# Optimization experiments

Measured on AMD Instinct MI355X. Metric: run time of the kernel, lower is better.

Reference implementation:

```python
import jax, jax.numpy as jnp
import numpy as np

N_NODES = 100_000
N_EDGES = 1_600_000
N_GRAPHS = 512
IN_C, HID_C, OUT_C = 17, 64, 32


def setup_inputs() -> dict:
    key = jax.random.key(0)
    ks = jax.random.split(key, 12)
    x = jax.random.normal(ks[0], (N_NODES, IN_C), dtype=jnp.float32)
    edge_index = jax.random.randint(ks[1], (2, N_EDGES), 0, N_NODES, dtype=jnp.int64)
    batch = jnp.sort(jax.random.randint(ks[2], (N_NODES,), 0, N_GRAPHS, dtype=jnp.int64))
    def lin(k, fan_in, fan_out):
        s = 1.0 / np.sqrt(fan_in)
        kw, kb = jax.random.split(k)
        W = jax.random.uniform(kw, (fan_in, fan_out), minval=-s, maxval=s, dtype=jnp.float32)
        b = jax.random.uniform(kb, (fan_out,), minval=-s, maxval=s, dtype=jnp.float32)
        return W, b
    W1, b1 = lin(ks[3], IN_C, HID_C)      # GCNConv 1
    W2, b2 = lin(ks[4], HID_C, OUT_C)     # GCNConv 2
    Wf1, bf1 = lin(ks[5], OUT_C, OUT_C)   # fc1
    Wf2, bf2 = lin(ks[6], OUT_C, OUT_C)   # fc2
    return {"x": x, "edge_index": edge_index, "batch": batch,
            "W1": W1, "b1": b1, "W2": W2, "b2": b2,
            "Wf1": Wf1, "bf1": bf1, "Wf2": Wf2, "bf2": bf2}


def _gcn_conv(x, src, dst, norm, W, b, n_nodes):
    # PyG GCNConv: h = x @ W; out_i = sum_{j->i} norm_ij * h_j; out += bias
    h = x @ W                                   # [N, d_out]
    msg = h[src] * norm[:, None]                # gather + scale [E+N, d_out]
    out = jax.ops.segment_sum(msg, dst, num_segments=n_nodes)
    return out + b


def reference(x, edge_index, batch, W1, b1, W2, b2, Wf1, bf1, Wf2, bf2):
    n = x.shape[0]
    loops = jnp.arange(n, dtype=edge_index.dtype)
    src = jnp.concatenate([edge_index[0], loops])  # add self loops
    dst = jnp.concatenate([edge_index[1], loops])
    # symmetric normalization: deg^-1/2[src] * deg^-1/2[dst]
    deg = jax.ops.segment_sum(jnp.ones_like(dst, dtype=x.dtype), dst, num_segments=n)
    dinv = jnp.where(deg > 0, 1.0 / jnp.sqrt(deg), 0.0)
    norm = dinv[src] * dinv[dst]

    h = jax.nn.relu(_gcn_conv(x, src, dst, norm, W1, b1, n))
    h = _gcn_conv(h, src, dst, norm, W2, b2, n)

    # global mean pool over graphs
    cnt = jax.ops.segment_sum(jnp.ones((n,), dtype=h.dtype), batch, num_segments=N_GRAPHS)
    pooled = jax.ops.segment_sum(h, batch, num_segments=N_GRAPHS) / jnp.clip(cnt, 1.0)[:, None]

    out = jax.nn.relu(pooled @ Wf1 + bf1)
    out = out @ Wf2 + bf2
    return out  # [N_GRAPHS, OUT_C]
```

## Files before the change

### kernel.cpp

```cpp
#include <hip/hip_runtime.h>

#define IN_C 17
#define HID  64
#define OUTC 32

#define CH   8192
#define TA   512
#define NBP  512
#define BCAP 5632
#define BS_BLKS 8

typedef __attribute__((ext_vector_type(2))) float f2;
typedef __attribute__((ext_vector_type(8))) short bf16x8;
typedef __attribute__((ext_vector_type(4))) float f32x4;
__device__ __forceinline__ f2 mkf2(float x, float y) { f2 r; r.x = x; r.y = y; return r; }

__device__ __forceinline__ unsigned short f2bf(float f) {
    unsigned u = __float_as_uint(f);
    u += 0x7fffu + ((u >> 16) & 1u);
    return (unsigned short)(u >> 16);
}
__device__ __forceinline__ float bflo(unsigned u) { return __uint_as_float(u << 16); }
__device__ __forceinline__ float bfhi(unsigned u) { return __uint_as_float(u & 0xffff0000u); }

__global__ __launch_bounds__(TA) void k_binA(const int* __restrict__ src,
        const int* __restrict__ dst, int E,
        int* __restrict__ outbuf, int* __restrict__ cntmat, int* __restrict__ offmat) {
    __shared__ int cnt[NBP];
    __shared__ int off[NBP];
    __shared__ int stage[CH];
    int t = threadIdx.x;
    long base = (long)blockIdx.x * CH;
    int nE = (int)(E - base); if (nE > CH) nE = CH;
    cnt[t] = 0;
    __syncthreads();
    int bk[16], pk[16], rk[16];
#pragma unroll
    for (int j = 0; j < 16; ++j) {
        int idx = t + j * TA;
        if (idx < nE) {
            long e = base + idx;
            int d = __builtin_nontemporal_load(&dst[e]);
            int s = __builtin_nontemporal_load(&src[e]);
            int b = d >> 8;
            bk[j] = b;
            pk[j] = s | ((d & 255) << 17);
            rk[j] = atomicAdd(&cnt[b], 1);
        } else bk[j] = -1;
    }
    __syncthreads();
    int c = cnt[t];
    off[t] = c;
    __syncthreads();
    int inc = c;
    for (int s = 1; s < NBP; s <<= 1) {
        int add = (t >= s) ? off[t - s] : 0;
        __syncthreads();
        inc += add; off[t] = inc;
        __syncthreads();
    }
    int excl = inc - c;
    __syncthreads();
    off[t] = excl;
    __syncthreads();
#pragma unroll
    for (int j = 0; j < 16; ++j)
        if (bk[j] >= 0) stage[off[bk[j]] + rk[j]] = pk[j];
    __syncthreads();
    for (int i = t; i < nE; i += TA) outbuf[base + i] = stage[i];
    cntmat[blockIdx.x * NBP + t] = c;
    offmat[blockIdx.x * NBP + t] = excl;
}

__global__ __launch_bounds__(NBP) void k_bsum1(const int* __restrict__ cntmat,
        int nblkA, int* __restrict__ part, float* __restrict__ pool, int poolN) {
    int t = threadIdx.x, b = blockIdx.x;
    int per = (nblkA + BS_BLKS - 1) / BS_BLKS;
    int i0 = b * per, i1 = min(i0 + per, nblkA);
    int s = 0;
    for (int i = i0; i < i1; ++i) s += cntmat[i * NBP + t];
    part[b * NBP + t] = s;
    for (int i = b * NBP + t; i < poolN; i += BS_BLKS * NBP) pool[i] = 0.f;
}

__global__ __launch_bounds__(NBP) void k_bsum2(const int* __restrict__ part,
        int* __restrict__ bbase, const float* __restrict__ W2,
        uint4* __restrict__ w2frag) {
    __shared__ int sh[NBP];
    int t = threadIdx.x;
    int s = 0;
#pragma unroll
    for (int i = 0; i < BS_BLKS; ++i) s += part[i * NBP + t];
    sh[t] = s;
    __syncthreads();
    int inc = s;
    for (int st = 1; st < NBP; st <<= 1) {
        int add = (t >= st) ? sh[t - st] : 0;
        __syncthreads();
        inc += add; sh[t] = inc;
        __syncthreads();
    }
    bbase[t] = inc - s;
    if (t < 256) {
        int f = t >> 6, l = t & 63;
        int kt = f >> 1, nt = f & 1;
        int kbase = kt * 32 + (l >> 4) * 8;
        int c = nt * 16 + (l & 15);
        unsigned short v[8];
#pragma unroll
        for (int j = 0; j < 8; ++j) v[j] = f2bf(W2[(kbase + j) * OUTC + c]);
        uint4 o;
        o.x = (unsigned)v[0] | ((unsigned)v[1] << 16);
        o.y = (unsigned)v[2] | ((unsigned)v[3] << 16);
        o.z = (unsigned)v[4] | ((unsigned)v[5] << 16);
        o.w = (unsigned)v[6] | ((unsigned)v[7] << 16);
        w2frag[f * 64 + l] = o;
    }
}

__global__ __launch_bounds__(TA) void k_binB(const int* __restrict__ outbuf,
        const int* __restrict__ cntmat, const int* __restrict__ offmat,
        const int* __restrict__ bbase, int nblkA, int N,
        int* __restrict__ csr, int2* __restrict__ meta,
        const float* __restrict__ x, unsigned* __restrict__ xs16h,
        unsigned short* __restrict__ xs17h) {
    __shared__ int segc[256], sego[256], segs[256];
    __shared__ int ndeg[256], noff[256];
    __shared__ int stage[BCAP];
    int t = threadIdx.x, b = blockIdx.x;
    if (t < 256) {
        int cc = 0, ss = 0;
        if (t < nblkA) { cc = cntmat[t * NBP + b]; ss = offmat[t * NBP + b]; }
        segc[t] = cc; segs[t] = ss; sego[t] = cc;
        ndeg[t] = 0;
    }
    __syncthreads();
    {
        int c = (t < 256) ? sego[t] : 0;
        int inc = c;
        for (int s = 1; s < 256; s <<= 1) {
            int add = (t < 256 && t >= s) ? sego[t - s] : 0;
            __syncthreads();
            if (t < 256) { inc += add; sego[t] = inc; }
            __syncthreads();
        }
        if (t < 256) sego[t] = inc - c;
    }
    __syncthreads();
    int wave = t >> 6, lane = t & 63;
    for (int i = wave; i < nblkA; i += TA / 64) {
        int c = segc[i], so = sego[i];
        long gs = (long)i * CH + segs[i];
        for (int l = lane; l < c; l += 64) {
            int p = so + l;
            if (p < BCAP) stage[p] = __builtin_nontemporal_load(&outbuf[gs + l]);
        }
    }
    __syncthreads();
    int T = sego[255] + segc[255];
    if (T > BCAP) T = BCAP;
    int mypk[11], myrk[11], ne = 0;
    for (int k = t; k < T; k += TA) {
        int p = stage[k];
        int l = (p >> 17) & 255;
        myrk[ne] = atomicAdd(&ndeg[l], 1);
        mypk[ne] = p;
        ne++;
    }
    __syncthreads();
    {
        int c = (t < 256) ? ndeg[t] : 0;
        if (t < 256) noff[t] = c;
        __syncthreads();
        int inc = c;
        for (int s = 1; s < 256; s <<= 1) {
            int add = (t < 256 && t >= s) ? noff[t - s] : 0;
            __syncthreads();
            if (t < 256) { inc += add; noff[t] = inc; }
            __syncthreads();
        }
        if (t < 256) noff[t] = inc - c;
    }
    __syncthreads();
    int gb = bbase[b];
    int n0 = b << 8;
    if (t < 256 && n0 + t < N) {
        int n = n0 + t;
        meta[n] = make_int2(gb + noff[t], ndeg[t]);
        float dinv = rsqrtf((float)(ndeg[t] + 1));
        const float* xr = x + (size_t)n * IN_C;
        unsigned* xo = xs16h + (size_t)n * 8;
#pragma unroll
        for (int w2 = 0; w2 < 8; ++w2) {
            unsigned lo = f2bf(xr[2 * w2] * dinv);
            unsigned hi = f2bf(xr[2 * w2 + 1] * dinv);
            xo[w2] = lo | (hi << 16);
        }
        xs17h[n] = f2bf(xr[16] * dinv);
    }
    for (int j = 0; j < ne; ++j) {
        int p = mypk[j];
        int l = (p >> 17) & 255;
        csr[gb + noff[l] + myrk[j]] = p & 0x1FFFF;
    }
}

__global__ __launch_bounds__(256) void k_gather1(
        const uint4* __restrict__ xs16v, const unsigned short* __restrict__ xs17h,
        const int* __restrict__ csr, const int2* __restrict__ meta,
        const float* __restrict__ W1, const float* __restrict__ b1,
        const uint4* __restrict__ w2frag, unsigned char* __restrict__ hs2b, int N) {
    __shared__ __align__(16) float aggx[16][20];
    __shared__ float dinv_sh[16];
    __shared__ __align__(16) float h1sh[16][68];

    int tid = threadIdx.x;
    int n0 = blockIdx.x * 16;
    int ch = tid & 63;
    float w1r[IN_C];
#pragma unroll
    for (int k = 0; k < IN_C; ++k) w1r[k] = W1[k * HID + ch];
    float b1v = b1[ch];

    int ln = tid >> 4, sl = tid & 15;
    int n = n0 + ln;
    f2 acc[8];
#pragma unroll
    for (int j = 0; j < 8; ++j) acc[j] = mkf2(0.f, 0.f);
    float a17 = 0.f;
    if (n < N) {
        int2 m = meta[n];
        int start = m.x, cnt = m.y, end = start + cnt;
        auto body = [&](int s) {
            uint4 v0 = xs16v[(size_t)s * 2];
            uint4 v1 = xs16v[(size_t)s * 2 + 1];
            acc[0] += mkf2(bflo(v0.x), bfhi(v0.x));
            acc[1] += mkf2(bflo(v0.y), bfhi(v0.y));
            acc[2] += mkf2(bflo(v0.z), bfhi(v0.z));
            acc[3] += mkf2(bflo(v0.w), bfhi(v0.w));
            acc[4] += mkf2(bflo(v1.x), bfhi(v1.x));
            acc[5] += mkf2(bflo(v1.y), bfhi(v1.y));
            acc[6] += mkf2(bflo(v1.z), bfhi(v1.z));
            acc[7] += mkf2(bflo(v1.w), bfhi(v1.w));
            a17 += bflo((unsigned)xs17h[s]);
        };
        for (int k = start + sl; k < end; k += 16)
            body(__builtin_nontemporal_load(&csr[k]));
        if (sl == 0) {
            body(n);
            dinv_sh[ln] = rsqrtf((float)(cnt + 1));
        }
    }
    float a[16];
#pragma unroll
    for (int j = 0; j < 8; ++j) { a[2 * j] = acc[j].x; a[2 * j + 1] = acc[j].y; }
#pragma unroll
    for (int j = 0; j < 8; ++j) {
        float tt = (sl & 8) ? a[j + 8] : a[j];
        float uu = (sl & 8) ? a[j] : a[j + 8];
        a[j] = tt + __shfl_xor(uu, 8);
    }
#pragma unroll
    for (int j = 0; j < 4; ++j) {
        float tt = (sl & 4) ? a[j + 4] : a[j];
        float uu = (sl & 4) ? a[j] : a[j + 4];
        a[j] = tt + __shfl_xor(uu, 4);
    }
#pragma unroll
    for (int j = 0; j < 2; ++j) {
        float tt = (sl & 2) ? a[j + 2] : a[j];
        float uu = (sl & 2) ? a[j] : a[j + 2];
        a[j] = tt + __shfl_xor(uu, 2);
    }
    {
        float tt = (sl & 1) ? a[1] : a[0];
        float uu = (sl & 1) ? a[0] : a[1];
        a[0] = tt + __shfl_xor(uu, 1);
    }
    a17 += __shfl_xor(a17, 1);
    a17 += __shfl_xor(a17, 2);
    a17 += __shfl_xor(a17, 4);
    a17 += __shfl_xor(a17, 8);
    aggx[ln][sl] = a[0];
    if (sl == 0) aggx[ln][16] = a17;
    __syncthreads();
    int s0 = tid >> 6;
#pragma unroll
    for (int rep = 0; rep < 4; ++rep) {
        int slot = s0 + rep * 4;
        int nn = n0 + slot;
        if (nn < N) {
            const float4* ap = (const float4*)aggx[slot];
            float4 A0 = ap[0], A1 = ap[1], A2 = ap[2], A3 = ap[3];
            float a16 = aggx[slot][16];
            float dot = A0.x * w1r[0]  + A0.y * w1r[1]  + A0.z * w1r[2]  + A0.w * w1r[3]
                      + A1.x * w1r[4]  + A1.y * w1r[5]  + A1.z * w1r[6]  + A1.w * w1r[7]
                      + A2.x * w1r[8]  + A2.y * w1r[9]  + A2.z * w1r[10] + A2.w * w1r[11]
                      + A3.x * w1r[12] + A3.y * w1r[13] + A3.z * w1r[14] + A3.w * w1r[15]
                      + a16  * w1r[16];
            float dv = dinv_sh[slot];
            h1sh[slot][ch] = dv * fmaxf(dv * dot + b1v, 0.f);
        }
    }
    __syncthreads();
    int wv = tid >> 6, l = tid & 63;
    if (wv < 2) {
        int row = l & 15, kq = l >> 4;
        const float4* hp = (const float4*)&h1sh[row][kq * 8];
        float4 f0v = hp[0], f1v = hp[1];
        const float4* hq = (const float4*)&h1sh[row][32 + kq * 8];
        float4 g0v = hq[0], g1v = hq[1];
        bf16x8 a0, a1;
        a0[0] = (short)f2bf(f0v.x); a0[1] = (short)f2bf(f0v.y);
        a0[2] = (short)f2bf(f0v.z); a0[3] = (short)f2bf(f0v.w);
        a0[4] = (short)f2bf(f1v.x); a0[5] = (short)f2bf(f1v.y);
        a0[6] = (short)f2bf(f1v.z); a0[7] = (short)f2bf(f1v.w);
        a1[0] = (short)f2bf(g0v.x); a1[1] = (short)f2bf(g0v.y);
        a1[2] = (short)f2bf(g0v.z); a1[3] = (short)f2bf(g0v.w);
        a1[4] = (short)f2bf(g1v.x); a1[5] = (short)f2bf(g1v.y);
        a1[6] = (short)f2bf(g1v.z); a1[7] = (short)f2bf(g1v.w);
        bf16x8 bA = *(const bf16x8*)&w2frag[(0 + wv) * 64 + l];
        bf16x8 bB = *(const bf16x8*)&w2frag[(2 + wv) * 64 + l];
        f32x4 d = {0.f, 0.f, 0.f, 0.f};
        d = __builtin_amdgcn_mfma_f32_16x16x32_bf16(a0, bA, d, 0, 0, 0);
        d = __builtin_amdgcn_mfma_f32_16x16x32_bf16(a1, bB, d, 0, 0, 0);
        int rbase = (l >> 4) * 4;
#pragma unroll
        for (int r = 0; r < 4; ++r) {
            int node = n0 + rbase + r;
            if (node < N) {
                unsigned pk = (unsigned)__builtin_amdgcn_cvt_pk_fp8_f32(d[r], 0.f, 0, false);
                hs2b[(size_t)node * 32 + wv * 16 + (l & 15)] = (unsigned char)(pk & 0xFFu);
            }
        }
    }
}

__global__ __launch_bounds__(256) void k_gather2(
        const uint4* __restrict__ hs2v, const int* __restrict__ csr,
        const int2* __restrict__ meta, const float* __restrict__ b2,
        const int* __restrict__ batch, float* pool, float* cntg, int N) {
    __shared__ __align__(16) float cont[16][OUTC];
    __shared__ int bsh[16];
    int tid = threadIdx.x;
    int n0 = blockIdx.x * 16;

    int ln = tid >> 4, sl = tid & 15;
    int n = n0 + ln;
    f2 acc[16];
#pragma unroll
    for (int j = 0; j < 16; ++j) acc[j] = mkf2(0.f, 0.f);
    float dinv = 0.f;
    if (n < N) {
        int2 m = meta[n];
        int start = m.x, cnt = m.y, end = start + cnt;
        dinv = rsqrtf((float)(cnt + 1));
        auto body = [&](int s) {
            const uint4* rp = hs2v + (size_t)s * 2;
            uint4 v0 = rp[0], v1 = rp[1];
            f2 t;
            t = __builtin_amdgcn_cvt_pk_f32_fp8((int)v0.x, false); acc[0]  += t;
            t = __builtin_amdgcn_cvt_pk_f32_fp8((int)v0.x, true);  acc[1]  += t;
            t = __builtin_amdgcn_cvt_pk_f32_fp8((int)v0.y, false); acc[2]  += t;
            t = __builtin_amdgcn_cvt_pk_f32_fp8((int)v0.y, true);  acc[3]  += t;
            t = __builtin_amdgcn_cvt_pk_f32_fp8((int)v0.z, false); acc[4]  += t;
            t = __builtin_amdgcn_cvt_pk_f32_fp8((int)v0.z, true);  acc[5]  += t;
            t = __builtin_amdgcn_cvt_pk_f32_fp8((int)v0.w, false); acc[6]  += t;
            t = __builtin_amdgcn_cvt_pk_f32_fp8((int)v0.w, true);  acc[7]  += t;
            t = __builtin_amdgcn_cvt_pk_f32_fp8((int)v1.x, false); acc[8]  += t;
            t = __builtin_amdgcn_cvt_pk_f32_fp8((int)v1.x, true);  acc[9]  += t;
            t = __builtin_amdgcn_cvt_pk_f32_fp8((int)v1.y, false); acc[10] += t;
            t = __builtin_amdgcn_cvt_pk_f32_fp8((int)v1.y, true);  acc[11] += t;
            t = __builtin_amdgcn_cvt_pk_f32_fp8((int)v1.z, false); acc[12] += t;
            t = __builtin_amdgcn_cvt_pk_f32_fp8((int)v1.z, true);  acc[13] += t;
            t = __builtin_amdgcn_cvt_pk_f32_fp8((int)v1.w, false); acc[14] += t;
            t = __builtin_amdgcn_cvt_pk_f32_fp8((int)v1.w, true);  acc[15] += t;
        };
        for (int k = start + sl; k < end; k += 16)
            body(__builtin_nontemporal_load(&csr[k]));
        if (sl == 0) body(n);
    }
    float a[32];
#pragma unroll
    for (int j = 0; j < 16; ++j) { a[2 * j] = acc[j].x; a[2 * j + 1] = acc[j].y; }
#pragma unroll
    for (int j = 0; j < 16; ++j) {
        float tt = (sl & 8) ? a[j + 16] : a[j];
        float uu = (sl & 8) ? a[j] : a[j + 16];
        a[j] = tt + __shfl_xor(uu, 8);
    }
#pragma unroll
    for (int j = 0; j < 8; ++j) {
        float tt = (sl & 4) ? a[j + 8] : a[j];
        float uu = (sl & 4) ? a[j] : a[j + 8];
        a[j] = tt + __shfl_xor(uu, 4);
    }
#pragma unroll
    for (int j = 0; j < 4; ++j) {
        float tt = (sl & 2) ? a[j + 4] : a[j];
        float uu = (sl & 2) ? a[j] : a[j + 4];
        a[j] = tt + __shfl_xor(uu, 2);
    }
#pragma unroll
    for (int j = 0; j < 2; ++j) {
        float tt = (sl & 1) ? a[j + 2] : a[j];
        float uu = (sl & 1) ? a[j] : a[j + 2];
        a[j] = tt + __shfl_xor(uu, 1);
    }
    if (n < N) {
        float c0 = dinv * a[0] + b2[2 * sl];
        float c1 = dinv * a[1] + b2[2 * sl + 1];
        *(float2*)&cont[ln][2 * sl] = make_float2(c0, c1);
        if (sl == 0) bsh[ln] = batch[n];
    } else {
        *(float2*)&cont[ln][2 * sl] = make_float2(0.f, 0.f);
        if (sl == 0) bsh[ln] = -1;
    }
    __syncthreads();
    if (tid < OUTC) {
        int c = tid;
        float run = 0.f; int cur = -1;
        for (int j = 0; j < 16; ++j) {
            int bj = bsh[j];
            if (bj < 0) continue;
            if (bj == cur) run += cont[j][c];
            else {
                if (cur >= 0) atomicAdd(&pool[(size_t)cur * OUTC + c], run);
                cur = bj; run = cont[j][c];
            }
        }
        if (cur >= 0) atomicAdd(&pool[(size_t)cur * OUTC + c], run);
        if (c == 0) {
            float crun = 0.f; cur = -1;
            for (int j = 0; j < 16; ++j) {
                int bj = bsh[j];
                if (bj < 0) continue;
                if (bj == cur) crun += 1.f;
                else {
                    if (cur >= 0) atomicAdd(&cntg[cur], crun);
                    cur = bj; crun = 1.f;
                }
            }
            if (cur >= 0) atomicAdd(&cntg[cur], crun);
        }
    }
}

__global__ void k_final(const float* __restrict__ pool, const float* __restrict__ cntg,
                        const float* __restrict__ Wf1, const float* __restrict__ bf1,
                        const float* __restrict__ Wf2, const float* __restrict__ bf2,
                        float* out, int G) {
    __shared__ float p[OUTC], t[OUTC];
    int g = blockIdx.x;
    int c = threadIdx.x;
    float csafe = fmaxf(cntg[g], 1.0f);
    p[c] = pool[g * OUTC + c] / csafe;
    __syncthreads();
    float acc = bf1[c];
#pragma unroll
    for (int k = 0; k < OUTC; ++k) acc += p[k] * Wf1[k * OUTC + c];
    t[c] = fmaxf(acc, 0.f);
    __syncthreads();
    float acc2 = bf2[c];
#pragma unroll
    for (int k = 0; k < OUTC; ++k) acc2 += t[k] * Wf2[k * OUTC + c];
    out[g * OUTC + c] = acc2;
}

extern "C" void kernel_launch(void* const* d_in, const int* in_sizes, int n_in,
                              void* d_out, int out_size, void* d_ws, size_t ws_size,
                              hipStream_t stream) {
    const float* x    = (const float*)d_in[0];
    const int*   ei   = (const int*)  d_in[1];
    const int*   batch= (const int*)  d_in[2];
    const float* W1   = (const float*)d_in[3];
    const float* b1   = (const float*)d_in[4];
    const float* W2   = (const float*)d_in[5];
    const float* b2   = (const float*)d_in[6];
    const float* Wf1  = (const float*)d_in[7];
    const float* bf1  = (const float*)d_in[8];
    const float* Wf2  = (const float*)d_in[9];
    const float* bf2  = (const float*)d_in[10];

    const int N = in_sizes[0] / IN_C;
    const int E = in_sizes[1] / 2;
    const int G = out_size / OUTC;
    const int* src = ei;
    const int* dst = ei + E;

    const int nblkA = (E + CH - 1) / CH;
    const int NB    = (N + 255) >> 8;

    char* w = (char*)d_ws;
    int*   csr      = (int*)w;   w += (size_t)E * sizeof(int);
    int2*  meta     = (int2*)w;  w += (size_t)N * sizeof(int2);
    unsigned* xs16h = (unsigned*)w; w += (size_t)N * 8 * sizeof(unsigned);
    unsigned char* hs2 = (unsigned char*)w; w += (size_t)N * 32;
    unsigned short* xs17h = (unsigned short*)w; w += (size_t)N * sizeof(unsigned short);
    w = (char*)(((size_t)w + 15) & ~(size_t)15);
    float* pool     = (float*)w; w += (size_t)G * OUTC * sizeof(float);
    float* cntg     = (float*)w; w += (size_t)G * sizeof(float);
    w = (char*)(((size_t)w + 15) & ~(size_t)15);
    int*   outbuf   = (int*)w;   w += (size_t)E * sizeof(int);
    int*   cntmat   = (int*)w;   w += (size_t)nblkA * NBP * sizeof(int);
    int*   offmat   = (int*)w;   w += (size_t)nblkA * NBP * sizeof(int);
    int*   bbase    = (int*)w;   w += NBP * sizeof(int);
    int*   part     = (int*)w;   w += BS_BLKS * NBP * sizeof(int);
    w = (char*)(((size_t)w + 15) & ~(size_t)15);
    uint4* w2frag   = (uint4*)w; w += 4 * 64 * sizeof(uint4);

    const int poolN = G * OUTC + G;

    k_binA<<<nblkA, TA, 0, stream>>>(src, dst, E, outbuf, cntmat, offmat);
    k_bsum1<<<BS_BLKS, NBP, 0, stream>>>(cntmat, nblkA, part, pool, poolN);
    k_bsum2<<<1, NBP, 0, stream>>>(part, bbase, W2, w2frag);
    k_binB<<<NB, TA, 0, stream>>>(outbuf, cntmat, offmat, bbase, nblkA, N,
                                  csr, meta, x, xs16h, xs17h);

    dim3 blk(256);
    k_gather1<<<(N + 15) / 16, blk, 0, stream>>>((const uint4*)xs16h, xs17h, csr, meta,
                                                 W1, b1, w2frag, hs2, N);

    k_gather2<<<(N + 15) / 16, blk, 0, stream>>>((const uint4*)hs2, csr, meta,
                                                 b2, batch, pool, cntg, N);

    k_final<<<G, OUTC, 0, stream>>>(pool, cntg, Wf1, bf1, Wf2, bf2, (float*)d_out, G);
}
```

Before: 121.1 us.

## Fold bucket-sum kernels into binning kernels and make gather kernels persistent

Removes the two small bucket-prefix kernels. Pool zeroing and W2 fragment packing move into k_binA, and each k_binB block computes its global base by summing cntmat columns for all lower buckets and reducing in shared memory. The gather kernels become grid-stride loops over 16-node tiles with a grid capped at 2048 blocks, so W1/W2 register loads are amortized across tiles. This trades two launches and their serialization for redundant column sums in every binB block (up to 196x391 reads per block) and fewer resident blocks to hide gather latency.

```diff
diff --git a/kernel.cpp b/kernel.cpp
--- a/kernel.cpp
+++ b/kernel.cpp
@@ -8,7 +8,7 @@
 #define TA   512
 #define NBP  512
 #define BCAP 5632
-#define BS_BLKS 8
+#define MAXG 2048
 
 typedef __attribute__((ext_vector_type(2))) float f2;
 typedef __attribute__((ext_vector_type(8))) short bf16x8;
@@ -25,11 +25,30 @@
 
 __global__ __launch_bounds__(TA) void k_binA(const int* __restrict__ src,
         const int* __restrict__ dst, int E,
-        int* __restrict__ outbuf, int* __restrict__ cntmat, int* __restrict__ offmat) {
+        int* __restrict__ outbuf, int* __restrict__ cntmat, int* __restrict__ offmat,
+        const float* __restrict__ W2, uint4* __restrict__ w2frag,
+        float* __restrict__ pool, int poolN) {
     __shared__ int cnt[NBP];
     __shared__ int off[NBP];
     __shared__ int stage[CH];
     int t = threadIdx.x;
+    for (int i = (int)(blockIdx.x * TA + t); i < poolN; i += (int)(gridDim.x * TA))
+        pool[i] = 0.f;
+    if (blockIdx.x == 0 && t < 256) {
+        int f = t >> 6, l = t & 63;
+        int kt = f >> 1, nt = f & 1;
+        int kbase = kt * 32 + (l >> 4) * 8;
+        int c = nt * 16 + (l & 15);
+        unsigned short v[8];
+#pragma unroll
+        for (int j = 0; j < 8; ++j) v[j] = f2bf(W2[(kbase + j) * OUTC + c]);
+        uint4 o;
+        o.x = (unsigned)v[0] | ((unsigned)v[1] << 16);
+        o.y = (unsigned)v[2] | ((unsigned)v[3] << 16);
+        o.z = (unsigned)v[4] | ((unsigned)v[5] << 16);
+        o.w = (unsigned)v[6] | ((unsigned)v[7] << 16);
+        w2frag[f * 64 + l] = o;
+    }
     long base = (long)blockIdx.x * CH;
     int nE = (int)(E - base); if (nE > CH) nE = CH;
     cnt[t] = 0;
@@ -72,62 +91,21 @@
     offmat[blockIdx.x * NBP + t] = excl;
 }
 
-__global__ __launch_bounds__(NBP) void k_bsum1(const int* __restrict__ cntmat,
-        int nblkA, int* __restrict__ part, float* __restrict__ pool, int poolN) {
-    int t = threadIdx.x, b = blockIdx.x;
-    int per = (nblkA + BS_BLKS - 1) / BS_BLKS;
-    int i0 = b * per, i1 = min(i0 + per, nblkA);
-    int s = 0;
-    for (int i = i0; i < i1; ++i) s += cntmat[i * NBP + t];
-    part[b * NBP + t] = s;
-    for (int i = b * NBP + t; i < poolN; i += BS_BLKS * NBP) pool[i] = 0.f;
-}
-
-__global__ __launch_bounds__(NBP) void k_bsum2(const int* __restrict__ part,
-        int* __restrict__ bbase, const float* __restrict__ W2,
-        uint4* __restrict__ w2frag) {
-    __shared__ int sh[NBP];
-    int t = threadIdx.x;
-    int s = 0;
-#pragma unroll
-    for (int i = 0; i < BS_BLKS; ++i) s += part[i * NBP + t];
-    sh[t] = s;
-    __syncthreads();
-    int inc = s;
-    for (int st = 1; st < NBP; st <<= 1) {
-        int add = (t >= st) ? sh[t - st] : 0;
-        __syncthreads();
-        inc += add; sh[t] = inc;
-        __syncthreads();
-    }
-    bbase[t] = inc - s;
-    if (t < 256) {
-        int f = t >> 6, l = t & 63;
-        int kt = f >> 1, nt = f & 1;
-        int kbase = kt * 32 + (l >> 4) * 8;
-        int c = nt * 16 + (l & 15);
-        unsigned short v[8];
-#pragma unroll
-        for (int j = 0; j < 8; ++j) v[j] = f2bf(W2[(kbase + j) * OUTC + c]);
-        uint4 o;
-        o.x = (unsigned)v[0] | ((unsigned)v[1] << 16);
-        o.y = (unsigned)v[2] | ((unsigned)v[3] << 16);
-        o.z = (unsigned)v[4] | ((unsigned)v[5] << 16);
-        o.w = (unsigned)v[6] | ((unsigned)v[7] << 16);
-        w2frag[f * 64 + l] = o;
-    }
-}
-
 __global__ __launch_bounds__(TA) void k_binB(const int* __restrict__ outbuf,
         const int* __restrict__ cntmat, const int* __restrict__ offmat,
-        const int* __restrict__ bbase, int nblkA, int N,
+        int nblkA, int N,
         int* __restrict__ csr, int2* __restrict__ meta,
         const float* __restrict__ x, unsigned* __restrict__ xs16h,
         unsigned short* __restrict__ xs17h) {
     __shared__ int segc[256], sego[256], segs[256];
     __shared__ int ndeg[256], noff[256];
+    __shared__ int red[TA];
     __shared__ int stage[BCAP];
     int t = threadIdx.x, b = blockIdx.x;
+    int colsum = 0;
+    if (t < b) {
+        for (int i = 0; i < nblkA; ++i) colsum += cntmat[i * NBP + t];
+    }
     if (t < 256) {
         int cc = 0, ss = 0;
         if (t < nblkA) { cc = cntmat[t * NBP + b]; ss = offmat[t * NBP + b]; }
@@ -182,7 +160,13 @@
         if (t < 256) noff[t] = inc - c;
     }
     __syncthreads();
-    int gb = bbase[b];
+    red[t] = colsum;
+    __syncthreads();
+    for (int s = TA / 2; s > 0; s >>= 1) {
+        if (t < s) red[t] += red[t + s];
+        __syncthreads();
+    }
+    int gb = red[0];
     int n0 = b << 8;
     if (t < 256 && n0 + t < N) {
         int n = n0 + t;
@@ -209,240 +193,248 @@
         const uint4* __restrict__ xs16v, const unsigned short* __restrict__ xs17h,
         const int* __restrict__ csr, const int2* __restrict__ meta,
         const float* __restrict__ W1, const float* __restrict__ b1,
-        const uint4* __restrict__ w2frag, unsigned char* __restrict__ hs2b, int N) {
+        const uint4* __restrict__ w2frag, unsigned char* __restrict__ hs2b,
+        int N, int ntiles) {
     __shared__ __align__(16) float aggx[16][20];
     __shared__ float dinv_sh[16];
     __shared__ __align__(16) float h1sh[16][68];
 
     int tid = threadIdx.x;
-    int n0 = blockIdx.x * 16;
     int ch = tid & 63;
     float w1r[IN_C];
 #pragma unroll
     for (int k = 0; k < IN_C; ++k) w1r[k] = W1[k * HID + ch];
     float b1v = b1[ch];
-
+    int wv = tid >> 6, l = tid & 63;
+    bf16x8 bA = *(const bf16x8*)&w2frag[(0 + (wv & 1)) * 64 + l];
+    bf16x8 bB = *(const bf16x8*)&w2frag[(2 + (wv & 1)) * 64 + l];
     int ln = tid >> 4, sl = tid & 15;
-    int n = n0 + ln;
-    f2 acc[8];
-#pragma unroll
-    for (int j = 0; j < 8; ++j) acc[j] = mkf2(0.f, 0.f);
-    float a17 = 0.f;
-    if (n < N) {
-        int2 m = meta[n];
-        int start = m.x, cnt = m.y, end = start + cnt;
-        auto body = [&](int s) {
-            uint4 v0 = xs16v[(size_t)s * 2];
-            uint4 v1 = xs16v[(size_t)s * 2 + 1];
-            acc[0] += mkf2(bflo(v0.x), bfhi(v0.x));
-            acc[1] += mkf2(bflo(v0.y), bfhi(v0.y));
-            acc[2] += mkf2(bflo(v0.z), bfhi(v0.z));
-            acc[3] += mkf2(bflo(v0.w), bfhi(v0.w));
-            acc[4] += mkf2(bflo(v1.x), bfhi(v1.x));
-            acc[5] += mkf2(bflo(v1.y), bfhi(v1.y));
-            acc[6] += mkf2(bflo(v1.z), bfhi(v1.z));
-            acc[7] += mkf2(bflo(v1.w), bfhi(v1.w));
-            a17 += bflo((unsigned)xs17h[s]);
-        };
-        for (int k = start + sl; k < end; k += 16)
-            body(__builtin_nontemporal_load(&csr[k]));
-        if (sl == 0) {
-            body(n);
-            dinv_sh[ln] = rsqrtf((float)(cnt + 1));
-        }
-    }
-    float a[16];
-#pragma unroll
-    for (int j = 0; j < 8; ++j) { a[2 * j] = acc[j].x; a[2 * j + 1] = acc[j].y; }
-#pragma unroll
-    for (int j = 0; j < 8; ++j) {
-        float tt = (sl & 8) ? a[j + 8] : a[j];
-        float uu = (sl & 8) ? a[j] : a[j + 8];
-        a[j] = tt + __shfl_xor(uu, 8);
-    }
-#pragma unroll
-    for (int j = 0; j < 4; ++j) {
-        float tt = (sl & 4) ? a[j + 4] : a[j];
-        float uu = (sl & 4) ? a[j] : a[j + 4];
-        a[j] = tt + __shfl_xor(uu, 4);
-    }
-#pragma unroll
-    for (int j = 0; j < 2; ++j) {
-        float tt = (sl & 2) ? a[j + 2] : a[j];
-        float uu = (sl & 2) ? a[j] : a[j + 2];
-        a[j] = tt + __shfl_xor(uu, 2);
-    }
-    {
-        float tt = (sl & 1) ? a[1] : a[0];
-        float uu = (sl & 1) ? a[0] : a[1];
-        a[0] = tt + __shfl_xor(uu, 1);
-    }
-    a17 += __shfl_xor(a17, 1);
-    a17 += __shfl_xor(a17, 2);
-    a17 += __shfl_xor(a17, 4);
-    a17 += __shfl_xor(a17, 8);
-    aggx[ln][sl] = a[0];
-    if (sl == 0) aggx[ln][16] = a17;
-    __syncthreads();
     int s0 = tid >> 6;
-#pragma unroll
-    for (int rep = 0; rep < 4; ++rep) {
-        int slot = s0 + rep * 4;
-        int nn = n0 + slot;
-        if (nn < N) {
-            const float4* ap = (const float4*)aggx[slot];
-            float4 A0 = ap[0], A1 = ap[1], A2 = ap[2], A3 = ap[3];
-            float a16 = aggx[slot][16];
-            float dot = A0.x * w1r[0]  + A0.y * w1r[1]  + A0.z * w1r[2]  + A0.w * w1r[3]
-                      + A1.x * w1r[4]  + A1.y * w1r[5]  + A1.z * w1r[6]  + A1.w * w1r[7]
-                      + A2.x * w1r[8]  + A2.y * w1r[9]  + A2.z * w1r[10] + A2.w * w1r[11]
-                      + A3.x * w1r[12] + A3.y * w1r[13] + A3.z * w1r[14] + A3.w * w1r[15]
-                      + a16  * w1r[16];
-            float dv = dinv_sh[slot];
-            h1sh[slot][ch] = dv * fmaxf(dv * dot + b1v, 0.f);
-        }
-    }
-    __syncthreads();
-    int wv = tid >> 6, l = tid & 63;
-    if (wv < 2) {
-        int row = l & 15, kq = l >> 4;
-        const float4* hp = (const float4*)&h1sh[row][kq * 8];
-        float4 f0v = hp[0], f1v = hp[1];
-        const float4* hq = (const float4*)&h1sh[row][32 + kq * 8];
-        float4 g0v = hq[0], g1v = hq[1];
-        bf16x8 a0, a1;
-        a0[0] = (short)f2bf(f0v.x); a0[1] = (short)f2bf(f0v.y);
-        a0[2] = (short)f2bf(f0v.z); a0[3] = (short)f2bf(f0v.w);
-        a0[4] = (short)f2bf(f1v.x); a0[5] = (short)f2bf(f1v.y);
-        a0[6] = (short)f2bf(f1v.z); a0[7] = (short)f2bf(f1v.w);
-        a1[0] = (short)f2bf(g0v.x); a1[1] = (short)f2bf(g0v.y);
-        a1[2] = (short)f2bf(g0v.z); a1[3] = (short)f2bf(g0v.w);
-        a1[4] = (short)f2bf(g1v.x); a1[5] = (short)f2bf(g1v.y);
-        a1[6] = (short)f2bf(g1v.z); a1[7] = (short)f2bf(g1v.w);
-        bf16x8 bA = *(const bf16x8*)&w2frag[(0 + wv) * 64 + l];
-        bf16x8 bB = *(const bf16x8*)&w2frag[(2 + wv) * 64 + l];
-        f32x4 d = {0.f, 0.f, 0.f, 0.f};
-        d = __builtin_amdgcn_mfma_f32_16x16x32_bf16(a0, bA, d, 0, 0, 0);
-        d = __builtin_amdgcn_mfma_f32_16x16x32_bf16(a1, bB, d, 0, 0, 0);
-        int rbase = (l >> 4) * 4;
-#pragma unroll
-        for (int r = 0; r < 4; ++r) {
-            int node = n0 + rbase + r;
-            if (node < N) {
-                unsigned pk = (unsigned)__builtin_amdgcn_cvt_pk_fp8_f32(d[r], 0.f, 0, false);
-                hs2b[(size_t)node * 32 + wv * 16 + (l & 15)] = (unsigned char)(pk & 0xFFu);
+
+    for (int tile = blockIdx.x; tile < ntiles; tile += gridDim.x) {
+        int n0 = tile * 16;
+        int n = n0 + ln;
+        f2 acc[8];
+#pragma unroll
+        for (int j = 0; j < 8; ++j) acc[j] = mkf2(0.f, 0.f);
+        float a17 = 0.f;
+        if (n < N) {
+            int2 m = meta[n];
+            int start = m.x, cnt = m.y, end = start + cnt;
+            auto body = [&](int s) {
+                uint4 v0 = xs16v[(size_t)s * 2];
+                uint4 v1 = xs16v[(size_t)s * 2 + 1];
+                acc[0] += mkf2(bflo(v0.x), bfhi(v0.x));
+                acc[1] += mkf2(bflo(v0.y), bfhi(v0.y));
+                acc[2] += mkf2(bflo(v0.z), bfhi(v0.z));
+                acc[3] += mkf2(bflo(v0.w), bfhi(v0.w));
+                acc[4] += mkf2(bflo(v1.x), bfhi(v1.x));
+                acc[5] += mkf2(bflo(v1.y), bfhi(v1.y));
+                acc[6] += mkf2(bflo(v1.z), bfhi(v1.z));
+                acc[7] += mkf2(bflo(v1.w), bfhi(v1.w));
+                a17 += bflo((unsigned)xs17h[s]);
+            };
+            for (int k = start + sl; k < end; k += 16)
+                body(__builtin_nontemporal_load(&csr[k]));
+            if (sl == 0) {
+                body(n);
+                dinv_sh[ln] = rsqrtf((float)(cnt + 1));
             }
         }
+        float a[16];
+#pragma unroll
+        for (int j = 0; j < 8; ++j) { a[2 * j] = acc[j].x; a[2 * j + 1] = acc[j].y; }
+#pragma unroll
+        for (int j = 0; j < 8; ++j) {
+            float tt = (sl & 8) ? a[j + 8] : a[j];
+            float uu = (sl & 8) ? a[j] : a[j + 8];
+            a[j] = tt + __shfl_xor(uu, 8);
+        }
+#pragma unroll
+        for (int j = 0; j < 4; ++j) {
+            float tt = (sl & 4) ? a[j + 4] : a[j];
+            float uu = (sl & 4) ? a[j] : a[j + 4];
+            a[j] = tt + __shfl_xor(uu, 4);
+        }
+#pragma unroll
+        for (int j = 0; j < 2; ++j) {
+            float tt = (sl & 2) ? a[j + 2] : a[j];
+            float uu = (sl & 2) ? a[j] : a[j + 2];
+            a[j] = tt + __shfl_xor(uu, 2);
+        }
+        {
+            float tt = (sl & 1) ? a[1] : a[0];
+            float uu = (sl & 1) ? a[0] : a[1];
+            a[0] = tt + __shfl_xor(uu, 1);
+        }
+        a17 += __shfl_xor(a17, 1);
+        a17 += __shfl_xor(a17, 2);
+        a17 += __shfl_xor(a17, 4);
+        a17 += __shfl_xor(a17, 8);
+        aggx[ln][sl] = a[0];
+        if (sl == 0) aggx[ln][16] = a17;
+        __syncthreads();
+#pragma unroll
+        for (int rep = 0; rep < 4; ++rep) {
+            int slot = s0 + rep * 4;
+            int nn = n0 + slot;
+            if (nn < N) {
+                const float4* ap = (const float4*)aggx[slot];
+                float4 A0 = ap[0], A1 = ap[1], A2 = ap[2], A3 = ap[3];
+                float a16 = aggx[slot][16];
+                float dot = A0.x * w1r[0]  + A0.y * w1r[1]  + A0.z * w1r[2]  + A0.w * w1r[3]
+                          + A1.x * w1r[4]  + A1.y * w1r[5]  + A1.z * w1r[6]  + A1.w * w1r[7]
+                          + A2.x * w1r[8]  + A2.y * w1r[9]  + A2.z * w1r[10] + A2.w * w1r[11]
+                          + A3.x * w1r[12] + A3.y * w1r[13] + A3.z * w1r[14] + A3.w * w1r[15]
+                          + a16  * w1r[16];
+                float dv = dinv_sh[slot];
+                h1sh[slot][ch] = dv * fmaxf(dv * dot + b1v, 0.f);
+            }
+        }
+        __syncthreads();
+        if (wv < 2) {
+            int row = l & 15, kq = l >> 4;
+            const float4* hp = (const float4*)&h1sh[row][kq * 8];
+            float4 f0v = hp[0], f1v = hp[1];
+            const float4* hq = (const float4*)&h1sh[row][32 + kq * 8];
+            float4 g0v = hq[0], g1v = hq[1];
+            bf16x8 a0, a1;
+            a0[0] = (short)f2bf(f0v.x); a0[1] = (short)f2bf(f0v.y);
+            a0[2] = (short)f2bf(f0v.z); a0[3] = (short)f2bf(f0v.w);
+            a0[4] = (short)f2bf(f1v.x); a0[5] = (short)f2bf(f1v.y);
+            a0[6] = (short)f2bf(f1v.z); a0[7] = (short)f2bf(f1v.w);
+            a1[0] = (short)f2bf(g0v.x); a1[1] = (short)f2bf(g0v.y);
+            a1[2] = (short)f2bf(g0v.z); a1[3] = (short)f2bf(g0v.w);
+            a1[4] = (short)f2bf(g1v.x); a1[5] = (short)f2bf(g1v.y);
+            a1[6] = (short)f2bf(g1v.z); a1[7] = (short)f2bf(g1v.w);
+            f32x4 d = {0.f, 0.f, 0.f, 0.f};
+            d = __builtin_amdgcn_mfma_f32_16x16x32_bf16(a0, bA, d, 0, 0, 0);
+            d = __builtin_amdgcn_mfma_f32_16x16x32_bf16(a1, bB, d, 0, 0, 0);
+            int rbase = (l >> 4) * 4;
+#pragma unroll
+            for (int r = 0; r < 4; ++r) {
+                int node = n0 + rbase + r;
+                if (node < N) {
+                    unsigned pk = (unsigned)__builtin_amdgcn_cvt_pk_fp8_f32(d[r], 0.f, 0, false);
+                    hs2b[(size_t)node * 32 + wv * 16 + (l & 15)] = (unsigned char)(pk & 0xFFu);
+                }
+            }
+        }
+        __syncthreads();
     }
 }
 
 __global__ __launch_bounds__(256) void k_gather2(
         const uint4* __restrict__ hs2v, const int* __restrict__ csr,
         const int2* __restrict__ meta, const float* __restrict__ b2,
-        const int* __restrict__ batch, float* pool, float* cntg, int N) {
+        const int* __restrict__ batch, float* pool, float* cntg,
+        int N, int ntiles) {
     __shared__ __align__(16) float cont[16][OUTC];
     __shared__ int bsh[16];
     int tid = threadIdx.x;
-    int n0 = blockIdx.x * 16;
-
     int ln = tid >> 4, sl = tid & 15;
-    int n = n0 + ln;
-    f2 acc[16];
-#pragma unroll
-    for (int j = 0; j < 16; ++j) acc[j] = mkf2(0.f, 0.f);
-    float dinv = 0.f;
-    if (n < N) {
-        int2 m = meta[n];
-        int start = m.x, cnt = m.y, end = start + cnt;
-        dinv = rsqrtf((float)(cnt + 1));
-        auto body = [&](int s) {
-            const uint4* rp = hs2v + (size_t)s * 2;
-            uint4 v0 = rp[0], v1 = rp[1];
-            f2 t;
-            t = __builtin_amdgcn_cvt_pk_f32_fp8((int)v0.x, false); acc[0]  += t;
-            t = __builtin_amdgcn_cvt_pk_f32_fp8((int)v0.x, true);  acc[1]  += t;
-            t = __builtin_amdgcn_cvt_pk_f32_fp8((int)v0.y, false); acc[2]  += t;
-            t = __builtin_amdgcn_cvt_pk_f32_fp8((int)v0.y, true);  acc[3]  += t;
-            t = __builtin_amdgcn_cvt_pk_f32_fp8((int)v0.z, false); acc[4]  += t;
-            t = __builtin_amdgcn_cvt_pk_f32_fp8((int)v0.z, true);  acc[5]  += t;
-            t = __builtin_amdgcn_cvt_pk_f32_fp8((int)v0.w, false); acc[6]  += t;
-            t = __builtin_amdgcn_cvt_pk_f32_fp8((int)v0.w, true);  acc[7]  += t;
-            t = __builtin_amdgcn_cvt_pk_f32_fp8((int)v1.x, false); acc[8]  += t;
-            t = __builtin_amdgcn_cvt_pk_f32_fp8((int)v1.x, true);  acc[9]  += t;
-            t = __builtin_amdgcn_cvt_pk_f32_fp8((int)v1.y, false); acc[10] += t;
-            t = __builtin_amdgcn_cvt_pk_f32_fp8((int)v1.y, true);  acc[11] += t;
-            t = __builtin_amdgcn_cvt_pk_f32_fp8((int)v1.z, false); acc[12] += t;
-            t = __builtin_amdgcn_cvt_pk_f32_fp8((int)v1.z, true);  acc[13] += t;
-            t = __builtin_amdgcn_cvt_pk_f32_fp8((int)v1.w, false); acc[14] += t;
-            t = __builtin_amdgcn_cvt_pk_f32_fp8((int)v1.w, true);  acc[15] += t;
-        };
-        for (int k = start + sl; k < end; k += 16)
-            body(__builtin_nontemporal_load(&csr[k]));
-        if (sl == 0) body(n);
-    }
-    float a[32];
-#pragma unroll
-    for (int j = 0; j < 16; ++j) { a[2 * j] = acc[j].x; a[2 * j + 1] = acc[j].y; }
-#pragma unroll
-    for (int j = 0; j < 16; ++j) {
-        float tt = (sl & 8) ? a[j + 16] : a[j];
-        float uu = (sl & 8) ? a[j] : a[j + 16];
-        a[j] = tt + __shfl_xor(uu, 8);
-    }
-#pragma unroll
-    for (int j = 0; j < 8; ++j) {
-        float tt = (sl & 4) ? a[j + 8] : a[j];
-        float uu = (sl & 4) ? a[j] : a[j + 8];
-        a[j] = tt + __shfl_xor(uu, 4);
-    }
-#pragma unroll
-    for (int j = 0; j < 4; ++j) {
-        float tt = (sl & 2) ? a[j + 4] : a[j];
-        float uu = (sl & 2) ? a[j] : a[j + 4];
-        a[j] = tt + __shfl_xor(uu, 2);
-    }
-#pragma unroll
-    for (int j = 0; j < 2; ++j) {
-        float tt = (sl & 1) ? a[j + 2] : a[j];
-        float uu = (sl & 1) ? a[j] : a[j + 2];
-        a[j] = tt + __shfl_xor(uu, 1);
-    }
-    if (n < N) {
-        float c0 = dinv * a[0] + b2[2 * sl];
-        float c1 = dinv * a[1] + b2[2 * sl + 1];
-        *(float2*)&cont[ln][2 * sl] = make_float2(c0, c1);
-        if (sl == 0) bsh[ln] = batch[n];
-    } else {
-        *(float2*)&cont[ln][2 * sl] = make_float2(0.f, 0.f);
-        if (sl == 0) bsh[ln] = -1;
-    }
-    __syncthreads();
-    if (tid < OUTC) {
-        int c = tid;
-        float run = 0.f; int cur = -1;
+
+    for (int tile = blockIdx.x; tile < ntiles; tile += gridDim.x) {
+        int n0 = tile * 16;
+        int n = n0 + ln;
+        f2 acc[16];
+#pragma unroll
+        for (int j = 0; j < 16; ++j) acc[j] = mkf2(0.f, 0.f);
+        float dinv = 0.f;
+        if (n < N) {
+            int2 m = meta[n];
+            int start = m.x, cnt = m.y, end = start + cnt;
+            dinv = rsqrtf((float)(cnt + 1));
+            auto body = [&](int s) {
+                const uint4* rp = hs2v + (size_t)s * 2;
+                uint4 v0 = rp[0], v1 = rp[1];
+                f2 t;
+                t = __builtin_amdgcn_cvt_pk_f32_fp8((int)v0.x, false); acc[0]  += t;
+                t = __builtin_amdgcn_cvt_pk_f32_fp8((int)v0.x, true);  acc[1]  += t;
+                t = __builtin_amdgcn_cvt_pk_f32_fp8((int)v0.y, false); acc[2]  += t;
+                t = __builtin_amdgcn_cvt_pk_f32_fp8((int)v0.y, true);  acc[3]  += t;
+                t = __builtin_amdgcn_cvt_pk_f32_fp8((int)v0.z, false); acc[4]  += t;
+                t = __builtin_amdgcn_cvt_pk_f32_fp8((int)v0.z, true);  acc[5]  += t;
+                t = __builtin_amdgcn_cvt_pk_f32_fp8((int)v0.w, false); acc[6]  += t;
+                t = __builtin_amdgcn_cvt_pk_f32_fp8((int)v0.w, true);  acc[7]  += t;
+                t = __builtin_amdgcn_cvt_pk_f32_fp8((int)v1.x, false); acc[8]  += t;
+                t = __builtin_amdgcn_cvt_pk_f32_fp8((int)v1.x, true);  acc[9]  += t;
+                t = __builtin_amdgcn_cvt_pk_f32_fp8((int)v1.y, false); acc[10] += t;
+                t = __builtin_amdgcn_cvt_pk_f32_fp8((int)v1.y, true);  acc[11] += t;
+                t = __builtin_amdgcn_cvt_pk_f32_fp8((int)v1.z, false); acc[12] += t;
+                t = __builtin_amdgcn_cvt_pk_f32_fp8((int)v1.z, true);  acc[13] += t;
+                t = __builtin_amdgcn_cvt_pk_f32_fp8((int)v1.w, false); acc[14] += t;
+                t = __builtin_amdgcn_cvt_pk_f32_fp8((int)v1.w, true);  acc[15] += t;
+            };
+            for (int k = start + sl; k < end; k += 16)
+                body(__builtin_nontemporal_load(&csr[k]));
+            if (sl == 0) body(n);
+        }
+        float a[32];
+#pragma unroll
+        for (int j = 0; j < 16; ++j) { a[2 * j] = acc[j].x; a[2 * j + 1] = acc[j].y; }
+#pragma unroll
         for (int j = 0; j < 16; ++j) {
-            int bj = bsh[j];
-            if (bj < 0) continue;
-            if (bj == cur) run += cont[j][c];
-            else {
-                if (cur >= 0) atomicAdd(&pool[(size_t)cur * OUTC + c], run);
-                cur = bj; run = cont[j][c];
-            }
-        }
-        if (cur >= 0) atomicAdd(&pool[(size_t)cur * OUTC + c], run);
-        if (c == 0) {
-            float crun = 0.f; cur = -1;
+            float tt = (sl & 8) ? a[j + 16] : a[j];
+            float uu = (sl & 8) ? a[j] : a[j + 16];
+            a[j] = tt + __shfl_xor(uu, 8);
+        }
+#pragma unroll
+        for (int j = 0; j < 8; ++j) {
+            float tt = (sl & 4) ? a[j + 8] : a[j];
+            float uu = (sl & 4) ? a[j] : a[j + 8];
+            a[j] = tt + __shfl_xor(uu, 4);
+        }
+#pragma unroll
+        for (int j = 0; j < 4; ++j) {
+            float tt = (sl & 2) ? a[j + 4] : a[j];
+            float uu = (sl & 2) ? a[j] : a[j + 4];
+            a[j] = tt + __shfl_xor(uu, 2);
+        }
+#pragma unroll
+        for (int j = 0; j < 2; ++j) {
+            float tt = (sl & 1) ? a[j + 2] : a[j];
+            float uu = (sl & 1) ? a[j] : a[j + 2];
+            a[j] = tt + __shfl_xor(uu, 1);
+        }
+        if (n < N) {
+            float c0 = dinv * a[0] + b2[2 * sl];
+            float c1 = dinv * a[1] + b2[2 * sl + 1];
+            *(float2*)&cont[ln][2 * sl] = make_float2(c0, c1);
+            if (sl == 0) bsh[ln] = batch[n];
+        } else {
+            *(float2*)&cont[ln][2 * sl] = make_float2(0.f, 0.f);
+            if (sl == 0) bsh[ln] = -1;
+        }
+        __syncthreads();
+        if (tid < OUTC) {
+            int c = tid;
+            float run = 0.f; int cur = -1;
             for (int j = 0; j < 16; ++j) {
                 int bj = bsh[j];
                 if (bj < 0) continue;
-                if (bj == cur) crun += 1.f;
+                if (bj == cur) run += cont[j][c];
                 else {
-                    if (cur >= 0) atomicAdd(&cntg[cur], crun);
-                    cur = bj; crun = 1.f;
+                    if (cur >= 0) atomicAdd(&pool[(size_t)cur * OUTC + c], run);
+                    cur = bj; run = cont[j][c];
                 }
             }
-            if (cur >= 0) atomicAdd(&cntg[cur], crun);
-        }
+            if (cur >= 0) atomicAdd(&pool[(size_t)cur * OUTC + c], run);
+            if (c == 0) {
+                float crun = 0.f; cur = -1;
+                for (int j = 0; j < 16; ++j) {
+                    int bj = bsh[j];
+                    if (bj < 0) continue;
+                    if (bj == cur) crun += 1.f;
+                    else {
+                        if (cur >= 0) atomicAdd(&cntg[cur], crun);
+                        cur = bj; crun = 1.f;
+                    }
+                }
+                if (cur >= 0) atomicAdd(&cntg[cur], crun);
+            }
+        }
+        __syncthreads();
     }
 }
 
@@ -504,25 +496,24 @@
     int*   outbuf   = (int*)w;   w += (size_t)E * sizeof(int);
     int*   cntmat   = (int*)w;   w += (size_t)nblkA * NBP * sizeof(int);
     int*   offmat   = (int*)w;   w += (size_t)nblkA * NBP * sizeof(int);
-    int*   bbase    = (int*)w;   w += NBP * sizeof(int);
-    int*   part     = (int*)w;   w += BS_BLKS * NBP * sizeof(int);
     w = (char*)(((size_t)w + 15) & ~(size_t)15);
     uint4* w2frag   = (uint4*)w; w += 4 * 64 * sizeof(uint4);
 
     const int poolN = G * OUTC + G;
-
-    k_binA<<<nblkA, TA, 0, stream>>>(src, dst, E, outbuf, cntmat, offmat);
-    k_bsum1<<<BS_BLKS, NBP, 0, stream>>>(cntmat, nblkA, part, pool, poolN);
-    k_bsum2<<<1, NBP, 0, stream>>>(part, bbase, W2, w2frag);
-    k_binB<<<NB, TA, 0, stream>>>(outbuf, cntmat, offmat, bbase, nblkA, N,
+    const int ntiles = (N + 15) / 16;
+    const int gg = ntiles < MAXG ? ntiles : MAXG;
+
+    k_binA<<<nblkA, TA, 0, stream>>>(src, dst, E, outbuf, cntmat, offmat,
+                                     W2, w2frag, pool, poolN);
+    k_binB<<<NB, TA, 0, stream>>>(outbuf, cntmat, offmat, nblkA, N,
                                   csr, meta, x, xs16h, xs17h);
 
     dim3 blk(256);
-    k_gather1<<<(N + 15) / 16, blk, 0, stream>>>((const uint4*)xs16h, xs17h, csr, meta,
-                                                 W1, b1, w2frag, hs2, N);
-
-    k_gather2<<<(N + 15) / 16, blk, 0, stream>>>((const uint4*)hs2, csr, meta,
-                                                 b2, batch, pool, cntg, N);
+    k_gather1<<<gg, blk, 0, stream>>>((const uint4*)xs16h, xs17h, csr, meta,
+                                      W1, b1, w2frag, hs2, N, ntiles);
+
+    k_gather2<<<gg, blk, 0, stream>>>((const uint4*)hs2, csr, meta,
+                                      b2, batch, pool, cntg, N, ntiles);
 
     k_final<<<G, OUTC, 0, stream>>>(pool, cntg, Wf1, bf1, Wf2, bf2, (float*)d_out, G);
 }
```

After: 156.0 us. 1.29x slower.
